# Performance work log

Measured on AMD Instinct MI355X. Metric: run time of the kernel, lower is better.

The kernel has to match this reference:

```python
import jax, jax.numpy as jnp
import numpy as np

N = 50000
E = 800000
D = 128

def setup_inputs() -> dict:
    key = jax.random.key(0)
    k1, k2, k3 = jax.random.split(key, 3)
    node_feat = jax.random.normal(k1, (N, D), dtype=jnp.float32)
    edge_index = jax.random.randint(k2, (2, E), 0, N, dtype=jnp.int64)
    edge_feat = jax.random.normal(k3, (E, D), dtype=jnp.float32)
    eps = jnp.zeros((1,), dtype=jnp.float32)
    return {"node_feat": node_feat, "edge_index": edge_index, "edge_feat": edge_feat, "eps": eps}

def reference(node_feat, edge_index, edge_feat, eps):
    src = edge_index[0]
    dst = edge_index[1]
    n = node_feat.shape[0]
    # gather source node feats, add edge feats, ReLU  -> (E, D)
    msg = jax.nn.relu(node_feat[src] + edge_feat)
    # scatter-sum aggregate to destination nodes -> (N, D)
    neigh = jax.ops.segment_sum(msg, dst, num_segments=n)
    rst = (1.0 + eps) * node_feat + neigh
    return rst
```

## Files before the change

### kernel.cpp

```cpp
#include <hip/hip_runtime.h>


#define D 128
#define DV2 64

__global__ void init_out_kernel(const float4* __restrict__ nf,
                                const float* __restrict__ eps,
                                float4* __restrict__ out, int n4) {
    int i = blockIdx.x * blockDim.x + threadIdx.x;
    if (i >= n4) return;
    float s = 1.0f + eps[0];
    float4 v = nf[i];
    v.x *= s; v.y *= s; v.z *= s; v.w *= s;
    out[i] = v;
}

__global__ void edge_scatter_kernel(const float4* __restrict__ nf,
                                    const float4* __restrict__ ef,
                                    const int* __restrict__ src,
                                    const int* __restrict__ dst,
                                    float* __restrict__ out, int E_) {
    int t = blockIdx.x * blockDim.x + threadIdx.x;
    int e = t >> 5;
    int c = t & 31;
    if (e >= E_) return;
    int s = src[e];
    int d = dst[e];
    float4 a = ef[(size_t)e * 32 + c];
    float4 b = nf[(size_t)s * 32 + c];
    float4 m;
    m.x = fmaxf(a.x + b.x, 0.0f);
    m.y = fmaxf(a.y + b.y, 0.0f);
    m.z = fmaxf(a.z + b.z, 0.0f);
    m.w = fmaxf(a.w + b.w, 0.0f);
    float* o = out + (size_t)d * D + c * 4;
    atomicAdd(o + 0, m.x);
    atomicAdd(o + 1, m.y);
    atomicAdd(o + 2, m.z);
    atomicAdd(o + 3, m.w);
}

__global__ void histogram_kernel(const int* __restrict__ dst, int* __restrict__ deg, int E_) {
    int e = blockIdx.x * blockDim.x + threadIdx.x;
    if (e >= E_) return;
    atomicAdd(&deg[dst[e]], 1);
}

__global__ void scan_kernel(const int* __restrict__ deg, int* __restrict__ offs,
                            int* __restrict__ cursor, int n) {
    __shared__ int wsum[16];
    __shared__ int sh_carry;
    __shared__ int sh_total;
    int t = threadIdx.x;
    int lane = t & 63;
    int w = t >> 6;
    if (t == 0) sh_carry = 0;
    __syncthreads();
    for (int base = 0; base < n; base += 1024) {
        int idx = base + t;
        int x = (idx < n) ? deg[idx] : 0;
        int v = x;
        #pragma unroll
        for (int off = 1; off < 64; off <<= 1) {
            int u = __shfl_up(v, off);
            if (lane >= off) v += u;
        }
        if (lane == 63) wsum[w] = v;
        __syncthreads();
        if (t == 0) {
            int r = 0;
            #pragma unroll
            for (int i = 0; i < 16; ++i) { int tv = wsum[i]; wsum[i] = r; r += tv; }
            sh_total = r;
        }
        __syncthreads();
        int c = sh_carry;
        int excl = wsum[w] + v - x;
        if (idx < n) {
            offs[idx] = c + excl;
            cursor[idx] = c + excl;
        }
        __syncthreads();
        if (t == 0) sh_carry = c + sh_total;
        __syncthreads();
    }
    if (t == 0) offs[n] = sh_carry;
}

__global__ void scatter_perm_kernel(const int* __restrict__ src, const int* __restrict__ dst,
                                    int* __restrict__ cursor,
                                    int* __restrict__ perm_src, int* __restrict__ perm_eid,
                                    int E_) {
    int e = blockIdx.x * blockDim.x + threadIdx.x;
    if (e >= E_) return;
    int d = dst[e];
    int pos = atomicAdd(&cursor[d], 1);
    perm_src[pos] = src[e];
    perm_eid[pos] = e;
}

__global__ void aggregate_kernel(const float2* __restrict__ nf,
                                 const float2* __restrict__ ef,
                                 const int* __restrict__ offs,
                                 const int* __restrict__ perm_src,
                                 const int* __restrict__ perm_eid,
                                 const float* __restrict__ eps,
                                 float2* __restrict__ out, int n) {
    int wid = (blockIdx.x * blockDim.x + threadIdx.x) >> 6;
    int lane = threadIdx.x & 63;
    if (wid >= n) return;
    int start = offs[wid];
    int end   = offs[wid + 1];
    float accx = 0.0f, accy = 0.0f;
    int i = start;
    for (; i + 1 < end; i += 2) {
        int s0 = perm_src[i],     e0 = perm_eid[i];
        int s1 = perm_src[i + 1], e1 = perm_eid[i + 1];
        float2 a0 = ef[(size_t)e0 * DV2 + lane];
        float2 b0 = nf[(size_t)s0 * DV2 + lane];
        float2 a1 = ef[(size_t)e1 * DV2 + lane];
        float2 b1 = nf[(size_t)s1 * DV2 + lane];
        accx += fmaxf(a0.x + b0.x, 0.0f) + fmaxf(a1.x + b1.x, 0.0f);
        accy += fmaxf(a0.y + b0.y, 0.0f) + fmaxf(a1.y + b1.y, 0.0f);
    }
    if (i < end) {
        int s0 = perm_src[i], e0 = perm_eid[i];
        float2 a0 = ef[(size_t)e0 * DV2 + lane];
        float2 b0 = nf[(size_t)s0 * DV2 + lane];
        accx += fmaxf(a0.x + b0.x, 0.0f);
        accy += fmaxf(a0.y + b0.y, 0.0f);
    }
    float sc = 1.0f + eps[0];
    float2 self = nf[(size_t)wid * DV2 + lane];
    float2 o;
    o.x = sc * self.x + accx;
    o.y = sc * self.y + accy;
    out[(size_t)wid * DV2 + lane] = o;
}

extern "C" void kernel_launch(void* const* d_in, const int* in_sizes, int n_in,
                              void* d_out, int out_size, void* d_ws, size_t ws_size,
                              hipStream_t stream) {
    const float* node_feat = (const float*)d_in[0];
    const int*   edge_index = (const int*)d_in[1];
    const float* edge_feat = (const float*)d_in[2];
    const float* eps = (const float*)d_in[3];
    float* out = (float*)d_out;

    int ND = in_sizes[0];
    int N_ = ND / D;
    int E_ = in_sizes[1] / 2;
    const int* src = edge_index;
    const int* dst = edge_index + E_;

    size_t need = ((size_t)2 * N_ + 1 + (size_t)2 * E_) * sizeof(int);
    if (ws_size < need) {
        int n4 = ND / 4;
        init_out_kernel<<<(n4 + 255) / 256, 256, 0, stream>>>(
            (const float4*)node_feat, eps, (float4*)out, n4);
        long long total = (long long)E_ * 32;
        int g2 = (int)((total + 255) / 256);
        edge_scatter_kernel<<<g2, 256, 0, stream>>>(
            (const float4*)node_feat, (const float4*)edge_feat, src, dst, out, E_);
        return;
    }

    int* cursor   = (int*)d_ws;
    int* offs     = cursor + N_;
    int* perm_src = offs + (N_ + 1);
    int* perm_eid = perm_src + E_;

    hipMemsetAsync(cursor, 0, (size_t)N_ * sizeof(int), stream);
    histogram_kernel<<<(E_ + 255) / 256, 256, 0, stream>>>(dst, cursor, E_);
    scan_kernel<<<1, 1024, 0, stream>>>(cursor, offs, cursor, N_);
    scatter_perm_kernel<<<(E_ + 255) / 256, 256, 0, stream>>>(
        src, dst, cursor, perm_src, perm_eid, E_);
    int waves_per_block = 4;
    int g = (N_ + waves_per_block - 1) / waves_per_block;
    aggregate_kernel<<<g, 256, 0, stream>>>(
        (const float2*)node_feat, (const float2*)edge_feat,
        offs, perm_src, perm_eid, eps, (float2*)out, N_);
}
```

Measured before the change: 711.3 us.

## Chunked single-pass scan, packed int2 permutation, float4 half-wave edge aggregation

The scan kernel now gives each of 1024 threads a contiguous chunk, so one block-level scan replaces the serialized 1024-element loop with its repeated barriers. The permutation stores src and edge id together as one int2, so each edge needs a single load. The aggregate kernel splits each wave into two halves that process alternating edges with float4 loads, then combines the halves with a cross-lane shuffle. This cuts scan latency and raises memory-level parallelism, at the cost of uncoalesced per-thread chunk reads in the scan and idle half-waves on low-degree nodes.

```diff
diff --git a/kernel.cpp b/kernel.cpp
--- a/kernel.cpp
+++ b/kernel.cpp
@@ -2,7 +2,6 @@
 
 
 #define D 128
-#define DV2 64
 
 __global__ void init_out_kernel(const float4* __restrict__ nf,
                                 const float* __restrict__ eps,
@@ -49,93 +48,106 @@
 __global__ void scan_kernel(const int* __restrict__ deg, int* __restrict__ offs,
                             int* __restrict__ cursor, int n) {
     __shared__ int wsum[16];
-    __shared__ int sh_carry;
-    __shared__ int sh_total;
     int t = threadIdx.x;
     int lane = t & 63;
     int w = t >> 6;
-    if (t == 0) sh_carry = 0;
+    int chunk = (n + 1023) >> 10;
+    int begin = t * chunk; if (begin > n) begin = n;
+    int endi = begin + chunk; if (endi > n) endi = n;
+
+    int s = 0;
+    for (int i = begin; i < endi; ++i) s += deg[i];
+
+    int v = s;
+    #pragma unroll
+    for (int off = 1; off < 64; off <<= 1) {
+        int u = __shfl_up(v, off);
+        if (lane >= off) v += u;
+    }
+    if (lane == 63) wsum[w] = v;
     __syncthreads();
-    for (int base = 0; base < n; base += 1024) {
-        int idx = base + t;
-        int x = (idx < n) ? deg[idx] : 0;
-        int v = x;
+    if (t == 0) {
+        int r = 0;
         #pragma unroll
-        for (int off = 1; off < 64; off <<= 1) {
-            int u = __shfl_up(v, off);
-            if (lane >= off) v += u;
-        }
-        if (lane == 63) wsum[w] = v;
-        __syncthreads();
-        if (t == 0) {
-            int r = 0;
-            #pragma unroll
-            for (int i = 0; i < 16; ++i) { int tv = wsum[i]; wsum[i] = r; r += tv; }
-            sh_total = r;
-        }
-        __syncthreads();
-        int c = sh_carry;
-        int excl = wsum[w] + v - x;
-        if (idx < n) {
-            offs[idx] = c + excl;
-            cursor[idx] = c + excl;
-        }
-        __syncthreads();
-        if (t == 0) sh_carry = c + sh_total;
-        __syncthreads();
+        for (int i = 0; i < 16; ++i) { int tv = wsum[i]; wsum[i] = r; r += tv; }
     }
-    if (t == 0) offs[n] = sh_carry;
+    __syncthreads();
+
+    int run = wsum[w] + v - s;
+    for (int i = begin; i < endi; ++i) {
+        int d = deg[i];
+        offs[i] = run;
+        cursor[i] = run;
+        run += d;
+    }
+    if (t == 1023) offs[n] = run;
 }
 
 __global__ void scatter_perm_kernel(const int* __restrict__ src, const int* __restrict__ dst,
                                     int* __restrict__ cursor,
-                                    int* __restrict__ perm_src, int* __restrict__ perm_eid,
-                                    int E_) {
+                                    int2* __restrict__ perm, int E_) {
     int e = blockIdx.x * blockDim.x + threadIdx.x;
     if (e >= E_) return;
     int d = dst[e];
     int pos = atomicAdd(&cursor[d], 1);
-    perm_src[pos] = src[e];
-    perm_eid[pos] = e;
+    perm[pos] = make_int2(src[e], e);
 }
 
-__global__ void aggregate_kernel(const float2* __restrict__ nf,
-                                 const float2* __restrict__ ef,
+__global__ void aggregate_kernel(const float4* __restrict__ nf,
+                                 const float4* __restrict__ ef,
                                  const int* __restrict__ offs,
-                                 const int* __restrict__ perm_src,
-                                 const int* __restrict__ perm_eid,
+                                 const int2* __restrict__ perm,
                                  const float* __restrict__ eps,
-                                 float2* __restrict__ out, int n) {
+                                 float4* __restrict__ out, int n) {
     int wid = (blockIdx.x * blockDim.x + threadIdx.x) >> 6;
+    if (wid >= n) return;
     int lane = threadIdx.x & 63;
-    if (wid >= n) return;
+    int half = lane >> 5;
+    int col  = lane & 31;
+
     int start = offs[wid];
     int end   = offs[wid + 1];
-    float accx = 0.0f, accy = 0.0f;
-    int i = start;
-    for (; i + 1 < end; i += 2) {
-        int s0 = perm_src[i],     e0 = perm_eid[i];
-        int s1 = perm_src[i + 1], e1 = perm_eid[i + 1];
-        float2 a0 = ef[(size_t)e0 * DV2 + lane];
-        float2 b0 = nf[(size_t)s0 * DV2 + lane];
-        float2 a1 = ef[(size_t)e1 * DV2 + lane];
-        float2 b1 = nf[(size_t)s1 * DV2 + lane];
+
+    float accx = 0.0f, accy = 0.0f, accz = 0.0f, accw = 0.0f;
+
+    int i = start + half;
+    for (; i + 2 < end; i += 4) {
+        int2 p0 = perm[i];
+        int2 p1 = perm[i + 2];
+        float4 a0 = ef[(size_t)p0.y * 32 + col];
+        float4 b0 = nf[(size_t)p0.x * 32 + col];
+        float4 a1 = ef[(size_t)p1.y * 32 + col];
+        float4 b1 = nf[(size_t)p1.x * 32 + col];
         accx += fmaxf(a0.x + b0.x, 0.0f) + fmaxf(a1.x + b1.x, 0.0f);
         accy += fmaxf(a0.y + b0.y, 0.0f) + fmaxf(a1.y + b1.y, 0.0f);
+        accz += fmaxf(a0.z + b0.z, 0.0f) + fmaxf(a1.z + b1.z, 0.0f);
+        accw += fmaxf(a0.w + b0.w, 0.0f) + fmaxf(a1.w + b1.w, 0.0f);
     }
-    if (i < end) {
-        int s0 = perm_src[i], e0 = perm_eid[i];
-        float2 a0 = ef[(size_t)e0 * DV2 + lane];
-        float2 b0 = nf[(size_t)s0 * DV2 + lane];
+    for (; i < end; i += 2) {
+        int2 p0 = perm[i];
+        float4 a0 = ef[(size_t)p0.y * 32 + col];
+        float4 b0 = nf[(size_t)p0.x * 32 + col];
         accx += fmaxf(a0.x + b0.x, 0.0f);
         accy += fmaxf(a0.y + b0.y, 0.0f);
+        accz += fmaxf(a0.z + b0.z, 0.0f);
+        accw += fmaxf(a0.w + b0.w, 0.0f);
     }
-    float sc = 1.0f + eps[0];
-    float2 self = nf[(size_t)wid * DV2 + lane];
-    float2 o;
-    o.x = sc * self.x + accx;
-    o.y = sc * self.y + accy;
-    out[(size_t)wid * DV2 + lane] = o;
+
+    accx += __shfl_xor(accx, 32);
+    accy += __shfl_xor(accy, 32);
+    accz += __shfl_xor(accz, 32);
+    accw += __shfl_xor(accw, 32);
+
+    if (half == 0) {
+        float sc = 1.0f + eps[0];
+        float4 self = nf[(size_t)wid * 32 + col];
+        float4 o;
+        o.x = sc * self.x + accx;
+        o.y = sc * self.y + accy;
+        o.z = sc * self.z + accz;
+        o.w = sc * self.w + accw;
+        out[(size_t)wid * 32 + col] = o;
+    }
 }
 
 extern "C" void kernel_launch(void* const* d_in, const int* in_sizes, int n_in,
@@ -153,7 +165,7 @@
     const int* src = edge_index;
     const int* dst = edge_index + E_;
 
-    size_t need = ((size_t)2 * N_ + 1 + (size_t)2 * E_) * sizeof(int);
+    size_t need = ((size_t)2 * N_ + 2) * sizeof(int) + (size_t)E_ * sizeof(int2);
     if (ws_size < need) {
         int n4 = ND / 4;
         init_out_kernel<<<(n4 + 255) / 256, 256, 0, stream>>>(
@@ -165,19 +177,18 @@
         return;
     }
 
-    int* cursor   = (int*)d_ws;
-    int* offs     = cursor + N_;
-    int* perm_src = offs + (N_ + 1);
-    int* perm_eid = perm_src + E_;
+    int* cursor = (int*)d_ws;
+    int* offs   = cursor + N_;
+    int2* perm  = (int2*)(offs + (N_ + 2));
 
     hipMemsetAsync(cursor, 0, (size_t)N_ * sizeof(int), stream);
     histogram_kernel<<<(E_ + 255) / 256, 256, 0, stream>>>(dst, cursor, E_);
     scan_kernel<<<1, 1024, 0, stream>>>(cursor, offs, cursor, N_);
     scatter_perm_kernel<<<(E_ + 255) / 256, 256, 0, stream>>>(
-        src, dst, cursor, perm_src, perm_eid, E_);
+        src, dst, cursor, perm, E_);
     int waves_per_block = 4;
     int g = (N_ + waves_per_block - 1) / waves_per_block;
     aggregate_kernel<<<g, 256, 0, stream>>>(
-        (const float2*)node_feat, (const float2*)edge_feat,
-        offs, perm_src, perm_eid, eps, (float2*)out, N_);
+        (const float4*)node_feat, (const float4*)edge_feat,
+        offs, perm, eps, (float4*)out, N_);
 }
```

Measured after the change: 760.1 us. +6.9%, slower.
